# Kernel tuning notes

Measured on AMD Instinct MI355X. Metric: run time of the kernel, lower is better.

The kernel has to match this reference:

```python
import jax, jax.numpy as jnp
import numpy as np

# config constants (init_kwargs)
WC, WS = 0.5, 0.5            # boundary cosine / structural weights (hybrid mode)
TARGET_BPP = 6.0             # target_bytes_per_patch
GAIN = 1.0                   # target_patch_gain
THRESH = 0.5                 # boundary_threshold; mask = p >= THRESH
EPS = 1e-6

_POP6 = jnp.array([bin(i).count('1') for i in range(64)], dtype=jnp.int32)

def _pop6(x):
    return _POP6[jnp.clip(x, 0, 63)]

def _logit(p):
    p = jnp.clip(p, EPS, 1.0 - EPS)
    return jnp.log(p) - jnp.log1p(-p)

def _next(x):  # shift-left by one, zero-padded at end (matches torch q_next pattern)
    return jnp.concatenate([x[1:], jnp.zeros((1,), x.dtype)])

def _hist(vals, mask, bins):
    idx = jnp.where(mask, vals, bins)  # invalid -> out of range, dropped
    return jnp.zeros((bins,), jnp.int32).at[idx].add(1, mode='drop')


def setup_inputs() -> dict:
    key = jax.random.key(0)
    ks = jax.random.split(key, 6)
    B, S = 4, 1048576
    return {
        'boundary_logprobs': jax.random.normal(ks[0], (B, S), jnp.float32),
        'states': jax.random.randint(ks[1], (B, S), 0, 4096, jnp.int32),
        'q_class': jax.random.randint(ks[2], (B, S), 0, 64, jnp.int32),
        'family': jax.random.randint(ks[3], (B, S), 0, 4, jnp.int32),
        'micro_ref': jax.random.randint(ks[4], (B, S), 0, 64, jnp.int32),
        'valid_mask': jax.random.randint(ks[5], (B, S), 0, 2, jnp.int32).astype(bool),
    }


def reference(boundary_logprobs, states, q_class, family, micro_ref, valid_mask):
    B, S = valid_mask.shape
    v = valid_mask.reshape(-1)
    st = states.reshape(-1).astype(jnp.int32)
    q = q_class.reshape(-1).astype(jnp.int32)
    fam = family.reshape(-1).astype(jnp.int32)
    mic = micro_ref.reshape(-1).astype(jnp.int32)

    # --- structural boundary probs ---
    omega12 = st & 0xFFF
    c6 = ((omega12 >> 6) ^ omega12) & 63          # chirality6
    d_chi = jnp.clip(_pop6(c6 ^ _next(c6)).astype(jnp.float32) / 6.0, 0.0, 1.0)
    d_q = _pop6((q & 63) ^ (_next(q) & 63)).astype(jnp.float32) / 6.0
    fx = (fam & 3) ^ (_next(fam) & 3)
    d_fam = (((fx & 1) != 0).astype(jnp.float32) + ((fx & 2) != 0).astype(jnp.float32)) / 2.0
    score = jnp.clip(0.5 * d_chi + 0.35 * d_q + 0.15 * d_fam, EPS, 1.0)
    structural = jnp.where(v, score, 0.0)

    # --- combine with cosine probs (hybrid mode) ---
    cosine = jnp.exp(jnp.minimum(boundary_logprobs.reshape(-1), 0.0))
    combined = (WC * cosine + WS * structural) / max(WC + WS, 1e-6)

    # --- target bytes-per-patch rate adjustment ---
    vf = v.astype(jnp.float32)
    vc = jnp.maximum(jnp.sum(vf), 1.0)
    cur = jnp.clip(jnp.sum(combined * vf) / vc, 1e-4, 1.0 - 1e-4)
    tgt = max(1e-4, min(1.0 - 1e-4, 1.0 / TARGET_BPP))
    shift = _logit(jnp.asarray(tgt, jnp.float32)) - _logit(cur)
    combined = jax.nn.sigmoid(_logit(combined) + GAIN * shift)
    combined = jnp.clip(combined, EPS, 1.0 - EPS)
    combined_logprobs = jnp.log(combined)
    bmask = combined_logprobs >= jnp.log(jnp.asarray(THRESH, jnp.float32))

    # --- histograms over effective (valid) positions ---
    shell = _pop6(c6)
    q_hist64 = _hist(q, v, 64)
    family_hist4 = _hist(fam, v, 4)
    micro_hist64 = _hist(mic, v, 64)
    shell_hist7 = _hist(shell, v, 7)
    wt_q = _pop6(q & 63)
    q_weight_hist7 = _hist(wt_q, v, 7)
    bits = ((q & 63)[:, None] >> jnp.arange(6)) & 1            # [n, 6]
    bit_excitation6 = jnp.sum(bits * v[:, None].astype(jnp.int32), axis=0)

    # --- patch lengths (vectorized run-length over valid bytes) ---
    bv = bmask & v
    pos = jnp.cumsum(v.astype(jnp.int32))                      # 1-indexed valid position
    bpos = jnp.where(bv, pos, 0)
    prev = jax.lax.cummax(jnp.concatenate([jnp.zeros((1,), jnp.int32), bpos[:-1]]))
    lengths = jnp.where(bv, pos - prev, 0)                     # dense run lengths at boundaries
    total_valid = pos[-1]
    trailing = total_valid - jax.lax.cummax(bpos)[-1]          # open trailing run
    patch_count = jnp.sum(bv).astype(jnp.int32) + (trailing > 0).astype(jnp.int32)

    return (combined_logprobs.reshape(B, S), bmask.reshape(B, S), structural.reshape(B, S),
            q_hist64, family_hist4, micro_hist64, shell_hist7, q_weight_hist7,
            bit_excitation6, lengths, trailing, patch_count)
```

## Files before the change

kernel.cpp:

```cpp
#include <hip/hip_runtime.h>

#define TPB 256
#define EPT 8
#define CHUNK (TPB * EPT)
#define P2T 1024
#define NSLICE 64

typedef unsigned long long ull;

__device__ __forceinline__ ull shfl_down_u64(ull x, int off) {
    unsigned lo = (unsigned)x, hi = (unsigned)(x >> 32);
    lo = __shfl_down(lo, off, 64);
    hi = __shfl_down(hi, off, 64);
    return ((ull)hi << 32) | lo;
}

__global__ __launch_bounds__(TPB, 4) void k_pass1(
    const float* __restrict__ blp, const int* __restrict__ st,
    const int* __restrict__ q, const int* __restrict__ fam,
    const int* __restrict__ mic, const int* __restrict__ vm,
    float* __restrict__ out_structural,
    int* __restrict__ blocksum_v, double* __restrict__ blocksum_c,
    int* __restrict__ ghist, int n)
{
    __shared__ int lh2[512];
    __shared__ int slhs[24];
    __shared__ int swv[4];
    __shared__ float swc[4];
    for (int t = threadIdx.x; t < 512; t += TPB) lh2[t] = 0;
    if (threadIdx.x < 24) slhs[threadIdx.x] = 0;
    __syncthreads();

    const int tid = threadIdx.x, lane = tid & 63, wave = tid >> 6;
    const long i0 = (long)blockIdx.x * CHUNK + (long)tid * EPT;
    const bool fast = ((long)(blockIdx.x + 1) * CHUNK <= n);

    int stv[9], qv[9], fv[9], micv[8], vmv[8];
    float bpv[8];
    if (fast) {
        const int4 sa = *(const int4*)(st + i0),  sb = *(const int4*)(st + i0 + 4);
        const int4 qa = *(const int4*)(q + i0),   qb = *(const int4*)(q + i0 + 4);
        const int4 fa = *(const int4*)(fam + i0), fb = *(const int4*)(fam + i0 + 4);
        const int4 ma = *(const int4*)(mic + i0), mb = *(const int4*)(mic + i0 + 4);
        const int4 va = *(const int4*)(vm + i0),  vb = *(const int4*)(vm + i0 + 4);
        const float4 ba = *(const float4*)(blp + i0), bb = *(const float4*)(blp + i0 + 4);
        int nst = __shfl_down(sa.x, 1, 64);
        int nq  = __shfl_down(qa.x, 1, 64);
        int nf  = __shfl_down(fa.x, 1, 64);
        if (lane == 63) {
            const long j = i0 + 8;
            nst = (j < n) ? st[j]  : 0;
            nq  = (j < n) ? q[j]   : 0;
            nf  = (j < n) ? fam[j] : 0;
        }
        stv[0]=sa.x; stv[1]=sa.y; stv[2]=sa.z; stv[3]=sa.w; stv[4]=sb.x; stv[5]=sb.y; stv[6]=sb.z; stv[7]=sb.w; stv[8]=nst;
        qv[0]=qa.x;  qv[1]=qa.y;  qv[2]=qa.z;  qv[3]=qa.w;  qv[4]=qb.x;  qv[5]=qb.y;  qv[6]=qb.z;  qv[7]=qb.w;  qv[8]=nq;
        fv[0]=fa.x;  fv[1]=fa.y;  fv[2]=fa.z;  fv[3]=fa.w;  fv[4]=fb.x;  fv[5]=fb.y;  fv[6]=fb.z;  fv[7]=fb.w;  fv[8]=nf;
        micv[0]=ma.x; micv[1]=ma.y; micv[2]=ma.z; micv[3]=ma.w; micv[4]=mb.x; micv[5]=mb.y; micv[6]=mb.z; micv[7]=mb.w;
        vmv[0]=va.x; vmv[1]=va.y; vmv[2]=va.z; vmv[3]=va.w; vmv[4]=vb.x; vmv[5]=vb.y; vmv[6]=vb.z; vmv[7]=vb.w;
        bpv[0]=ba.x; bpv[1]=ba.y; bpv[2]=ba.z; bpv[3]=ba.w; bpv[4]=bb.x; bpv[5]=bb.y; bpv[6]=bb.z; bpv[7]=bb.w;
    } else {
        #pragma unroll
        for (int e = 0; e < 8; ++e) {
            long ii = i0 + e;
            bool r = ii < n;
            stv[e] = r ? st[ii] : 0;  qv[e] = r ? q[ii] : 0;  fv[e] = r ? fam[ii] : 0;
            micv[e] = r ? mic[ii] : 0; vmv[e] = r ? vm[ii] : 0; bpv[e] = r ? blp[ii] : 0.f;
        }
        stv[8] = (i0 + 8 < n) ? st[i0 + 8] : 0;
        qv[8]  = (i0 + 8 < n) ? q[i0 + 8] : 0;
        fv[8]  = (i0 + 8 < n) ? fam[i0 + 8] : 0;
    }

    int sv = 0;
    float scf = 0.0f;
    ull accF = 0, accS0 = 0, accS1 = 0, accW0 = 0, accW1 = 0, accB = 0;
    float structural[8];
    #pragma unroll
    for (int e = 0; e < 8; ++e) {
        int sti = stv[e], qi = qv[e], fi = fv[e], mi = micv[e];
        int v = (vmv[e] != 0);
        int om  = sti & 0xFFF;      int c6  = ((om  >> 6) ^ om ) & 63;
        int omn = stv[e+1] & 0xFFF; int c6n = ((omn >> 6) ^ omn) & 63;
        float d_chi = (float)__popc(c6 ^ c6n) * (1.0f / 6.0f);
        float d_q   = (float)__popc((qi & 63) ^ (qv[e+1] & 63)) * (1.0f / 6.0f);
        int fx = (fi & 3) ^ (fv[e+1] & 3);
        float d_fam = (float)((fx & 1) + ((fx >> 1) & 1)) * 0.5f;
        float score = 0.5f * d_chi + 0.35f * d_q + 0.15f * d_fam;
        score = fminf(fmaxf(score, 1e-6f), 1.0f);
        structural[e] = v ? score : 0.0f;
        float cosine = expf(fminf(bpv[e], 0.0f));
        float combined = 0.5f * (cosine + structural[e]);
        if (v) {
            sv += 1;
            scf += combined;
            atomicAdd(&lh2[(wave << 6) + (qi & 63)], 1);
            atomicAdd(&lh2[256 + (wave << 6) + (mi & 63)], 1);
            accF += 1ULL << ((fi & 3) * 16);
            int sh = __popc(c6);
            ull ts = 1ULL << ((sh & 3) * 16);
            if (sh < 4) accS0 += ts; else accS1 += ts;
            int wq = __popc(qi & 63);
            ull tw = 1ULL << ((wq & 3) * 16);
            if (wq < 4) accW0 += tw; else accW1 += tw;
            accB += ((ull)(qi & 63) * 0x0000201008040201ULL) & 0x0004010040100401ULL;
        }
    }

    if (fast) {
        float4 o;
        o.x=structural[0]; o.y=structural[1]; o.z=structural[2]; o.w=structural[3];
        *(float4*)(out_structural + i0) = o;
        o.x=structural[4]; o.y=structural[5]; o.z=structural[6]; o.w=structural[7];
        *(float4*)(out_structural + i0 + 4) = o;
    } else {
        #pragma unroll
        for (int e = 0; e < 8; ++e)
            if (i0 + e < n) out_structural[i0 + e] = structural[e];
    }

    #pragma unroll
    for (int off = 32; off > 0; off >>= 1) {
        sv  += __shfl_down(sv, off, 64);
        scf += __shfl_down(scf, off, 64);
        accF  += shfl_down_u64(accF, off);
        accS0 += shfl_down_u64(accS0, off);
        accS1 += shfl_down_u64(accS1, off);
        accW0 += shfl_down_u64(accW0, off);
        accW1 += shfl_down_u64(accW1, off);
        accB  += shfl_down_u64(accB, off);
    }
    if (lane == 0) {
        swv[wave] = sv; swc[wave] = scf;
        #pragma unroll
        for (int b2 = 0; b2 < 4; ++b2) atomicAdd(&slhs[b2],      (int)((accF  >> (16*b2)) & 0xFFFF));
        #pragma unroll
        for (int b2 = 0; b2 < 4; ++b2) atomicAdd(&slhs[4 + b2],  (int)((accS0 >> (16*b2)) & 0xFFFF));
        #pragma unroll
        for (int b2 = 0; b2 < 3; ++b2) atomicAdd(&slhs[8 + b2],  (int)((accS1 >> (16*b2)) & 0xFFFF));
        #pragma unroll
        for (int b2 = 0; b2 < 4; ++b2) atomicAdd(&slhs[11 + b2], (int)((accW0 >> (16*b2)) & 0xFFFF));
        #pragma unroll
        for (int b2 = 0; b2 < 3; ++b2) atomicAdd(&slhs[15 + b2], (int)((accW1 >> (16*b2)) & 0xFFFF));
        #pragma unroll
        for (int b2 = 0; b2 < 6; ++b2) atomicAdd(&slhs[18 + b2], (int)((accB  >> (10*b2)) & 0x3FF));
    }
    __syncthreads();
    if (tid == 0) {
        blocksum_v[blockIdx.x] = swv[0] + swv[1] + swv[2] + swv[3];
        blocksum_c[blockIdx.x] = (double)swc[0] + (double)swc[1] + (double)swc[2] + (double)swc[3];
    }
    int* gh = ghist + (blockIdx.x & (NSLICE - 1)) * 152;
    for (int t2 = tid; t2 < 152; t2 += TPB) {
        int val;
        if (t2 < 64)        val = lh2[t2] + lh2[64 + t2] + lh2[128 + t2] + lh2[192 + t2];
        else if (t2 < 68)   val = slhs[t2 - 64];
        else if (t2 < 132) { int b2 = t2 - 68; val = lh2[256 + b2] + lh2[320 + b2] + lh2[384 + b2] + lh2[448 + b2]; }
        else if (t2 < 139)  val = slhs[4 + (t2 - 132)];
        else if (t2 < 146)  val = slhs[11 + (t2 - 139)];
        else                val = slhs[18 + (t2 - 146)];
        if (val) atomicAdd(&gh[t2], val);
    }
}

__global__ __launch_bounds__(P2T) void k_pass2(
    const int* __restrict__ bsv, const double* __restrict__ bsc, int nb,
    int* __restrict__ pos_offset, float* __restrict__ shiftp,
    int* __restrict__ totalv_p, const int* __restrict__ ghist,
    float* __restrict__ out_hist)
{
    __shared__ int s[P2T];
    __shared__ double d[P2T];
    int t = threadIdx.x;
    int c0 = 2 * t, c1 = 2 * t + 1;
    int v0 = (c0 < nb) ? bsv[c0] : 0;
    int v1 = (c1 < nb) ? bsv[c1] : 0;
    double x0 = (c0 < nb) ? bsc[c0] : 0.0;
    double x1 = (c1 < nb) ? bsc[c1] : 0.0;
    s[t] = v0 + v1; d[t] = x0 + x1;
    __syncthreads();
    for (int off = 1; off < P2T; off <<= 1) {
        int add = (t >= off) ? s[t - off] : 0;
        __syncthreads();
        s[t] += add;
        __syncthreads();
    }
    if (c0 < nb) pos_offset[c0] = s[t] - v0 - v1;
    if (c1 < nb) pos_offset[c1] = s[t] - v1;
    for (int off = P2T / 2; off > 0; off >>= 1) {
        if (t < off) d[t] += d[t + off];
        __syncthreads();
    }
    if (t == 0) {
        int total_v = s[P2T - 1];
        *totalv_p = total_v;
        double vc = (double)(total_v > 1 ? total_v : 1);
        float cur = (float)(d[0] / vc);
        cur = fminf(fmaxf(cur, 1e-4f), 0.9999f);
        float p = fminf(fmaxf(cur, 1e-6f), 0.999999f);
        float lc = logf(p) - log1pf(-p);
        float tgt = (float)(1.0 / 6.0);
        float lt = logf(tgt) - log1pf(-tgt);
        *shiftp = lt - lc;
    }
    if (t < 152) {
        int acc = 0;
        #pragma unroll 8
        for (int sl = 0; sl < NSLICE; ++sl) acc += ghist[sl * 152 + t];
        out_hist[t] = (float)acc;
    }
}

__global__ __launch_bounds__(TPB, 8) void k_pass3(
    const float* __restrict__ strc, const float* __restrict__ blp,
    const float* __restrict__ shiftp, const int* __restrict__ pos_offset,
    float* __restrict__ out_logp, float* __restrict__ out_bmask,
    float* __restrict__ out_len, int* __restrict__ chunk_cnt,
    int* __restrict__ chunk_last, ull* __restrict__ chunk_first, int n)
{
    __shared__ int swt[4], swm[4], scnt[4];
    __shared__ ull sfirst[4];
    const int tid = threadIdx.x, lane = tid & 63, wave = tid >> 6;
    const long i0 = (long)blockIdx.x * CHUNK + (long)tid * EPT;
    const bool fast = ((long)(blockIdx.x + 1) * CHUNK <= n);
    const float shift = *shiftp;

    float sv8[8], bp8[8];
    if (fast) {
        const float4 s0 = *(const float4*)(strc + i0), s1 = *(const float4*)(strc + i0 + 4);
        const float4 p0 = *(const float4*)(blp + i0),  p1 = *(const float4*)(blp + i0 + 4);
        sv8[0]=s0.x; sv8[1]=s0.y; sv8[2]=s0.z; sv8[3]=s0.w; sv8[4]=s1.x; sv8[5]=s1.y; sv8[6]=s1.z; sv8[7]=s1.w;
        bp8[0]=p0.x; bp8[1]=p0.y; bp8[2]=p0.z; bp8[3]=p0.w; bp8[4]=p1.x; bp8[5]=p1.y; bp8[6]=p1.z; bp8[7]=p1.w;
    } else {
        #pragma unroll
        for (int e = 0; e < 8; ++e) {
            long ii = i0 + e;
            bool r = ii < n;
            sv8[e] = r ? strc[ii] : 0.0f;
            bp8[e] = r ? blp[ii] : 0.0f;
        }
    }

    unsigned mv = 0, mb = 0;
    float lp[8], bmf[8], lenv[8];
    #pragma unroll
    for (int e = 0; e < 8; ++e) {
        float s = sv8[e];
        int v = (s > 0.0f);
        float cosine = expf(fminf(bp8[e], 0.0f));
        float comb = 0.5f * (cosine + s);
        float p = fminf(fmaxf(comb, 1e-6f), 0.999999f);
        float z = logf(p) - log1pf(-p) + shift;
        float sgm = 1.0f / (1.0f + expf(-z));
        sgm = fminf(fmaxf(sgm, 1e-6f), 0.999999f);
        float clp = logf(sgm);
        lp[e] = clp;
        int bm = (clp >= -0.69314718f) ? 1 : 0;
        bmf[e] = (float)bm;
        mv |= (unsigned)v << e;
        if (bm & v) mb |= 1u << e;
        lenv[e] = 0.0f;
    }
    if (fast) {
        float4 o;
        o.x=lp[0]; o.y=lp[1]; o.z=lp[2]; o.w=lp[3];     *(float4*)(out_logp + i0) = o;
        o.x=lp[4]; o.y=lp[5]; o.z=lp[6]; o.w=lp[7];     *(float4*)(out_logp + i0 + 4) = o;
        o.x=bmf[0]; o.y=bmf[1]; o.z=bmf[2]; o.w=bmf[3]; *(float4*)(out_bmask + i0) = o;
        o.x=bmf[4]; o.y=bmf[5]; o.z=bmf[6]; o.w=bmf[7]; *(float4*)(out_bmask + i0 + 4) = o;
    } else {
        #pragma unroll
        for (int e = 0; e < 8; ++e)
            if (i0 + e < n) { out_logp[i0 + e] = lp[e]; out_bmask[i0 + e] = bmf[e]; }
    }

    int tvc = __popc(mv);
    int x = tvc;
    #pragma unroll
    for (int off = 1; off < 64; off <<= 1) {
        int y = __shfl_up(x, off, 64);
        if (lane >= off) x += y;
    }
    if (lane == 63) swt[wave] = x;
    __syncthreads();
    int wb = pos_offset[blockIdx.x];
    for (int w2 = 0; w2 < wave; ++w2) wb += swt[w2];
    const int vbase = wb + (x - tvc);

    int last = -1;
    if (mb) {
        int hb = 31 - __clz(mb);
        last = vbase + __popc(mv & ((2u << hb) - 1));
    }
    int m = last;
    #pragma unroll
    for (int off = 1; off < 64; off <<= 1) {
        int y = __shfl_up(m, off, 64);
        if (lane >= off && y > m) m = y;
    }
    int exm = __shfl_up(m, 1, 64);
    if (lane == 0) exm = -1;
    if (lane == 63) swm[wave] = m;
    int cnt = __popc(mb);
    ull fp = ~0ULL;
    if (mb) {
        int lb = __ffs(mb) - 1;
        int fv2 = vbase + __popc(mv & ((2u << lb) - 1));
        fp = ((ull)(unsigned)(i0 + lb) << 32) | (unsigned)fv2;
    }
    #pragma unroll
    for (int off = 32; off > 0; off >>= 1) {
        cnt += __shfl_down(cnt, off, 64);
        ull fo = shfl_down_u64(fp, off);
        if (fo < fp) fp = fo;
    }
    if (lane == 0) { scnt[wave] = cnt; sfirst[wave] = fp; }
    __syncthreads();

    int prev = exm;
    for (int w2 = 0; w2 < wave; ++w2) if (swm[w2] > prev) prev = swm[w2];
    int runv = 0;
    #pragma unroll
    for (int e = 0; e < 8; ++e) {
        runv += (mv >> e) & 1;
        if ((mb >> e) & 1) {
            int pos = vbase + runv;
            lenv[e] = (prev >= 0) ? (float)(pos - prev) : 0.0f;
            prev = pos;
        }
    }
    if (fast) {
        float4 o;
        o.x=lenv[0]; o.y=lenv[1]; o.z=lenv[2]; o.w=lenv[3]; *(float4*)(out_len + i0) = o;
        o.x=lenv[4]; o.y=lenv[5]; o.z=lenv[6]; o.w=lenv[7]; *(float4*)(out_len + i0 + 4) = o;
    } else {
        #pragma unroll
        for (int e = 0; e < 8; ++e)
            if (i0 + e < n) out_len[i0 + e] = lenv[e];
    }
    if (tid == 0) {
        int c = scnt[0] + scnt[1] + scnt[2] + scnt[3];
        int L = swm[0];
        if (swm[1] > L) L = swm[1];
        if (swm[2] > L) L = swm[2];
        if (swm[3] > L) L = swm[3];
        ull F = sfirst[0];
        if (sfirst[1] < F) F = sfirst[1];
        if (sfirst[2] < F) F = sfirst[2];
        if (sfirst[3] < F) F = sfirst[3];
        chunk_cnt[blockIdx.x] = c;
        chunk_last[blockIdx.x] = L > 0 ? L : 0;
        chunk_first[blockIdx.x] = F;
    }
}

__global__ __launch_bounds__(P2T) void k_pass4(
    const int* __restrict__ chunk_cnt, const int* __restrict__ chunk_last,
    const ull* __restrict__ chunk_first, const int* __restrict__ totalv_p,
    int nb, float* __restrict__ out_len,
    float* __restrict__ out_trailing, float* __restrict__ out_patch)
{
    __shared__ int s[P2T];
    __shared__ int cs[P2T];
    int t = threadIdx.x;
    int c0 = 2 * t, c1 = 2 * t + 1;
    int a = 0, b = 0;
    if (c0 < nb) { int z = chunk_last[c0]; a = z > 0 ? z : 0; }
    if (c1 < nb) { int z = chunk_last[c1]; b = z > 0 ? z : 0; }
    int cnt = ((c0 < nb) ? chunk_cnt[c0] : 0) + ((c1 < nb) ? chunk_cnt[c1] : 0);
    s[t] = a > b ? a : b;
    cs[t] = cnt;
    __syncthreads();
    for (int off = 1; off < P2T; off <<= 1) {
        int y = (t >= off) ? s[t - off] : 0;
        __syncthreads();
        if (y > s[t]) s[t] = y;
        __syncthreads();
    }
    int excl = (t > 0) ? s[t - 1] : 0;
    int carry0 = excl;
    int carry1 = excl > a ? excl : a;
    if (c0 < nb) {
        ull F = chunk_first[c0];
        if (F != ~0ULL) {
            int fi = (int)(F >> 32);
            int fv2 = (int)(F & 0xFFFFFFFFu);
            out_len[fi] = (float)(fv2 - carry0);
        }
    }
    if (c1 < nb) {
        ull F = chunk_first[c1];
        if (F != ~0ULL) {
            int fi = (int)(F >> 32);
            int fv2 = (int)(F & 0xFFFFFFFFu);
            out_len[fi] = (float)(fv2 - carry1);
        }
    }
    int gmax = s[P2T - 1];
    __syncthreads();
    for (int off = P2T / 2; off > 0; off >>= 1) {
        if (t < off) cs[t] += cs[t + off];
        __syncthreads();
    }
    if (t == 0) {
        int total_v = *totalv_p;
        int trailing = total_v - gmax;
        int patch = cs[0] + (trailing > 0 ? 1 : 0);
        *out_trailing = (float)trailing;
        *out_patch = (float)patch;
    }
}

extern "C" void kernel_launch(void* const* d_in, const int* in_sizes, int n_in,
                              void* d_out, int out_size, void* d_ws, size_t ws_size,
                              hipStream_t stream)
{
    const float* blp = (const float*)d_in[0];
    const int* st   = (const int*)d_in[1];
    const int* q    = (const int*)d_in[2];
    const int* fam  = (const int*)d_in[3];
    const int* mic  = (const int*)d_in[4];
    const int* vm   = (const int*)d_in[5];
    const int n = in_sizes[0];
    const int nb = (n + CHUNK - 1) / CHUNK;

    float* out = (float*)d_out;
    float* out_logp       = out;
    float* out_bmask      = out + (size_t)n;
    float* out_structural = out + 2 * (size_t)n;
    float* out_hist       = out + 3 * (size_t)n;
    float* out_len        = out + 3 * (size_t)n + 152;
    float* out_trailing   = out + 4 * (size_t)n + 152;
    float* out_patch      = out + 4 * (size_t)n + 153;

    char* w = (char*)d_ws;
    int*    ghist      = (int*)(w);
    int*    blocksum_v = (int*)(w + 40960);
    int*    pos_offset = (int*)(w + 57344);
    int*    chunk_cnt  = (int*)(w + 73728);
    int*    chunk_last = (int*)(w + 90112);
    float*  shiftp     = (float*)(w + 106496);
    int*    totalv_p   = (int*)(w + 106500);
    double* blocksum_c = (double*)(w + 110592);
    ull*    chunk_first= (ull*)(w + 131072);

    hipMemsetAsync(ghist, 0, NSLICE * 152 * 4, stream);

    k_pass1<<<dim3(nb), dim3(TPB), 0, stream>>>(
        blp, st, q, fam, mic, vm, out_structural,
        blocksum_v, blocksum_c, ghist, n);

    k_pass2<<<dim3(1), dim3(P2T), 0, stream>>>(
        blocksum_v, blocksum_c, nb, pos_offset, shiftp, totalv_p,
        ghist, out_hist);

    k_pass3<<<dim3(nb), dim3(TPB), 0, stream>>>(
        out_structural, blp, shiftp, pos_offset, out_logp, out_bmask,
        out_len, chunk_cnt, chunk_last, chunk_first, n);

    k_pass4<<<dim3(1), dim3(P2T), 0, stream>>>(
        chunk_cnt, chunk_last, chunk_first, totalv_p, nb, out_len,
        out_trailing, out_patch);
}
```

Baseline: 194.5 us.

## Fold single-block scan passes into last-block and decoupled-lookback logic

```diff
diff --git a/kernel.cpp b/kernel.cpp
--- a/kernel.cpp
+++ b/kernel.cpp
@@ -3,7 +3,6 @@
 #define TPB 256
 #define EPT 8
 #define CHUNK (TPB * EPT)
-#define P2T 1024
 #define NSLICE 64
 
 typedef unsigned long long ull;
@@ -14,21 +13,35 @@
     hi = __shfl_down(hi, off, 64);
     return ((ull)hi << 32) | lo;
 }
+__device__ __forceinline__ int aload32(int* p) {
+    return __hip_atomic_load(p, __ATOMIC_RELAXED, __HIP_MEMORY_SCOPE_AGENT);
+}
+__device__ __forceinline__ ull aload64(ull* p) {
+    return __hip_atomic_load(p, __ATOMIC_RELAXED, __HIP_MEMORY_SCOPE_AGENT);
+}
+__device__ __forceinline__ void astore64(ull* p, ull v) {
+    __hip_atomic_store(p, v, __ATOMIC_RELAXED, __HIP_MEMORY_SCOPE_AGENT);
+}
 
 __global__ __launch_bounds__(TPB, 4) void k_pass1(
     const float* __restrict__ blp, const int* __restrict__ st,
     const int* __restrict__ q, const int* __restrict__ fam,
     const int* __restrict__ mic, const int* __restrict__ vm,
     float* __restrict__ out_structural,
-    int* __restrict__ blocksum_v, double* __restrict__ blocksum_c,
-    int* __restrict__ ghist, int n)
+    int* __restrict__ bsum_v, ull* __restrict__ bsum_c,
+    int* __restrict__ ghist, int* __restrict__ ctrl,
+    int* __restrict__ pos_offset, float* __restrict__ shiftp,
+    int* __restrict__ totalv_p, float* __restrict__ out_hist, int n, int nb)
 {
     __shared__ int lh2[512];
-    __shared__ int slhs[24];
+    __shared__ int slhs[11];
     __shared__ int swv[4];
     __shared__ float swc[4];
+    __shared__ int sLast;
+    __shared__ int escan[TPB];
+    __shared__ double edbl[TPB];
     for (int t = threadIdx.x; t < 512; t += TPB) lh2[t] = 0;
-    if (threadIdx.x < 24) slhs[threadIdx.x] = 0;
+    if (threadIdx.x < 11) slhs[threadIdx.x] = 0;
     __syncthreads();
 
     const int tid = threadIdx.x, lane = tid & 63, wave = tid >> 6;
@@ -74,7 +87,7 @@
 
     int sv = 0;
     float scf = 0.0f;
-    ull accF = 0, accS0 = 0, accS1 = 0, accW0 = 0, accW1 = 0, accB = 0;
+    ull accF = 0, accS0 = 0, accS1 = 0;
     float structural[8];
     #pragma unroll
     for (int e = 0; e < 8; ++e) {
@@ -100,10 +113,6 @@
             int sh = __popc(c6);
             ull ts = 1ULL << ((sh & 3) * 16);
             if (sh < 4) accS0 += ts; else accS1 += ts;
-            int wq = __popc(qi & 63);
-            ull tw = 1ULL << ((wq & 3) * 16);
-            if (wq < 4) accW0 += tw; else accW1 += tw;
-            accB += ((ull)(qi & 63) * 0x0000201008040201ULL) & 0x0004010040100401ULL;
         }
     }
 
@@ -126,76 +135,75 @@
         accF  += shfl_down_u64(accF, off);
         accS0 += shfl_down_u64(accS0, off);
         accS1 += shfl_down_u64(accS1, off);
-        accW0 += shfl_down_u64(accW0, off);
-        accW1 += shfl_down_u64(accW1, off);
-        accB  += shfl_down_u64(accB, off);
     }
     if (lane == 0) {
         swv[wave] = sv; swc[wave] = scf;
         #pragma unroll
-        for (int b2 = 0; b2 < 4; ++b2) atomicAdd(&slhs[b2],      (int)((accF  >> (16*b2)) & 0xFFFF));
-        #pragma unroll
-        for (int b2 = 0; b2 < 4; ++b2) atomicAdd(&slhs[4 + b2],  (int)((accS0 >> (16*b2)) & 0xFFFF));
-        #pragma unroll
-        for (int b2 = 0; b2 < 3; ++b2) atomicAdd(&slhs[8 + b2],  (int)((accS1 >> (16*b2)) & 0xFFFF));
-        #pragma unroll
-        for (int b2 = 0; b2 < 4; ++b2) atomicAdd(&slhs[11 + b2], (int)((accW0 >> (16*b2)) & 0xFFFF));
-        #pragma unroll
-        for (int b2 = 0; b2 < 3; ++b2) atomicAdd(&slhs[15 + b2], (int)((accW1 >> (16*b2)) & 0xFFFF));
-        #pragma unroll
-        for (int b2 = 0; b2 < 6; ++b2) atomicAdd(&slhs[18 + b2], (int)((accB  >> (10*b2)) & 0x3FF));
+        for (int b2 = 0; b2 < 4; ++b2) atomicAdd(&slhs[b2],     (int)((accF  >> (16*b2)) & 0xFFFF));
+        #pragma unroll
+        for (int b2 = 0; b2 < 4; ++b2) atomicAdd(&slhs[4 + b2], (int)((accS0 >> (16*b2)) & 0xFFFF));
+        #pragma unroll
+        for (int b2 = 0; b2 < 3; ++b2) atomicAdd(&slhs[8 + b2], (int)((accS1 >> (16*b2)) & 0xFFFF));
     }
     __syncthreads();
     if (tid == 0) {
-        blocksum_v[blockIdx.x] = swv[0] + swv[1] + swv[2] + swv[3];
-        blocksum_c[blockIdx.x] = (double)swc[0] + (double)swc[1] + (double)swc[2] + (double)swc[3];
+        int bv = swv[0] + swv[1] + swv[2] + swv[3];
+        double bc = (double)swc[0] + (double)swc[1] + (double)swc[2] + (double)swc[3];
+        atomicExch(&bsum_v[blockIdx.x], bv);
+        atomicExch(&bsum_c[blockIdx.x], __double_as_longlong(bc));
     }
     int* gh = ghist + (blockIdx.x & (NSLICE - 1)) * 152;
-    for (int t2 = tid; t2 < 152; t2 += TPB) {
+    for (int t2 = tid; t2 < 139; t2 += TPB) {
         int val;
         if (t2 < 64)        val = lh2[t2] + lh2[64 + t2] + lh2[128 + t2] + lh2[192 + t2];
         else if (t2 < 68)   val = slhs[t2 - 64];
-        else if (t2 < 132) { int b2 = t2 - 68; val = lh2[256 + b2] + lh2[320 + b2] + lh2[384 + b2] + lh2[448 + b2]; }
-        else if (t2 < 139)  val = slhs[4 + (t2 - 132)];
-        else if (t2 < 146)  val = slhs[11 + (t2 - 139)];
-        else                val = slhs[18 + (t2 - 146)];
+        else if (t2 < 132) { int b2 = t2 - 68; val = lh2[128 + 128 + b2] + lh2[256 + 64 + b2] + lh2[384 + b2] + lh2[448 + b2]; }
+        else                val = slhs[4 + (t2 - 132)];
         if (val) atomicAdd(&gh[t2], val);
     }
-}
-
-__global__ __launch_bounds__(P2T) void k_pass2(
-    const int* __restrict__ bsv, const double* __restrict__ bsc, int nb,
-    int* __restrict__ pos_offset, float* __restrict__ shiftp,
-    int* __restrict__ totalv_p, const int* __restrict__ ghist,
-    float* __restrict__ out_hist)
-{
-    __shared__ int s[P2T];
-    __shared__ double d[P2T];
-    int t = threadIdx.x;
-    int c0 = 2 * t, c1 = 2 * t + 1;
-    int v0 = (c0 < nb) ? bsv[c0] : 0;
-    int v1 = (c1 < nb) ? bsv[c1] : 0;
-    double x0 = (c0 < nb) ? bsc[c0] : 0.0;
-    double x1 = (c1 < nb) ? bsc[c1] : 0.0;
-    s[t] = v0 + v1; d[t] = x0 + x1;
-    __syncthreads();
-    for (int off = 1; off < P2T; off <<= 1) {
-        int add = (t >= off) ? s[t - off] : 0;
+
+    __syncthreads();
+    if (tid == 0) sLast = (atomicAdd(&ctrl[0], 1) == nb - 1);
+    __syncthreads();
+    if (!sLast) return;
+
+    const int G = (nb + TPB - 1) / TPB;
+    int myv[16];
+    int msum = 0;
+    double myd = 0.0;
+    for (int g = 0; g < G; ++g) {
+        int j = tid * G + g;
+        int v = 0;
+        if (j < nb) {
+            v = aload32(&bsum_v[j]);
+            myd += __longlong_as_double(aload64(&bsum_c[j]));
+        }
+        myv[g] = v;
+        msum += v;
+    }
+    escan[tid] = msum;
+    edbl[tid] = myd;
+    __syncthreads();
+    for (int off = 1; off < TPB; off <<= 1) {
+        int add = (tid >= off) ? escan[tid - off] : 0;
         __syncthreads();
-        s[t] += add;
+        escan[tid] += add;
         __syncthreads();
     }
-    if (c0 < nb) pos_offset[c0] = s[t] - v0 - v1;
-    if (c1 < nb) pos_offset[c1] = s[t] - v1;
-    for (int off = P2T / 2; off > 0; off >>= 1) {
-        if (t < off) d[t] += d[t + off];
+    int run = escan[tid] - msum;
+    for (int g = 0; g < G; ++g) {
+        int j = tid * G + g;
+        if (j < nb) { pos_offset[j] = run; run += myv[g]; }
+    }
+    for (int off = TPB / 2; off > 0; off >>= 1) {
+        if (tid < off) edbl[tid] += edbl[tid + off];
         __syncthreads();
     }
-    if (t == 0) {
-        int total_v = s[P2T - 1];
+    if (tid == 0) {
+        int total_v = escan[TPB - 1];
         *totalv_p = total_v;
         double vc = (double)(total_v > 1 ? total_v : 1);
-        float cur = (float)(d[0] / vc);
+        float cur = (float)(edbl[0] / vc);
         cur = fminf(fmaxf(cur, 1e-4f), 0.9999f);
         float p = fminf(fmaxf(cur, 1e-6f), 0.999999f);
         float lc = logf(p) - log1pf(-p);
@@ -203,11 +211,23 @@
         float lt = logf(tgt) - log1pf(-tgt);
         *shiftp = lt - lc;
     }
-    if (t < 152) {
+    for (int t2 = tid; t2 < 139; t2 += TPB) {
         int acc = 0;
         #pragma unroll 8
-        for (int sl = 0; sl < NSLICE; ++sl) acc += ghist[sl * 152 + t];
-        out_hist[t] = (float)acc;
+        for (int sl = 0; sl < NSLICE; ++sl) acc += aload32(&ghist[sl * 152 + t2]);
+        out_hist[t2] = (float)acc;
+        if (t2 < 64) lh2[t2] = acc;
+    }
+    __syncthreads();
+    if (tid < 7) {
+        int s = 0;
+        for (int b = 0; b < 64; ++b) if (__popc(b) == tid) s += lh2[b];
+        out_hist[139 + tid] = (float)s;
+    }
+    if (tid < 6) {
+        int s = 0;
+        for (int b = 0; b < 64; ++b) s += lh2[b] * ((b >> tid) & 1);
+        out_hist[146 + tid] = (float)s;
     }
 }
 
@@ -215,14 +235,16 @@
     const float* __restrict__ strc, const float* __restrict__ blp,
     const float* __restrict__ shiftp, const int* __restrict__ pos_offset,
     float* __restrict__ out_logp, float* __restrict__ out_bmask,
-    float* __restrict__ out_len, int* __restrict__ chunk_cnt,
-    int* __restrict__ chunk_last, ull* __restrict__ chunk_first, int n)
+    float* __restrict__ out_len, ull* __restrict__ desc,
+    int* __restrict__ ctrl, const int* __restrict__ totalv_p,
+    float* __restrict__ out_trailing, float* __restrict__ out_patch, int n, int nb)
 {
     __shared__ int swt[4], swm[4], scnt[4];
-    __shared__ ull sfirst[4];
+    __shared__ int scarry, sLast;
     const int tid = threadIdx.x, lane = tid & 63, wave = tid >> 6;
-    const long i0 = (long)blockIdx.x * CHUNK + (long)tid * EPT;
-    const bool fast = ((long)(blockIdx.x + 1) * CHUNK <= n);
+    const int b = blockIdx.x;
+    const long i0 = (long)b * CHUNK + (long)tid * EPT;
+    const bool fast = ((long)(b + 1) * CHUNK <= n);
     const float shift = *shiftp;
 
     float sv8[8], bp8[8];
@@ -282,7 +304,7 @@
     }
     if (lane == 63) swt[wave] = x;
     __syncthreads();
-    int wb = pos_offset[blockIdx.x];
+    int wb = pos_offset[b];
     for (int w2 = 0; w2 < wave; ++w2) wb += swt[w2];
     const int vbase = wb + (x - tvc);
 
@@ -301,30 +323,45 @@
     if (lane == 0) exm = -1;
     if (lane == 63) swm[wave] = m;
     int cnt = __popc(mb);
-    ull fp = ~0ULL;
-    if (mb) {
-        int lb = __ffs(mb) - 1;
-        int fv2 = vbase + __popc(mv & ((2u << lb) - 1));
-        fp = ((ull)(unsigned)(i0 + lb) << 32) | (unsigned)fv2;
-    }
-    #pragma unroll
-    for (int off = 32; off > 0; off >>= 1) {
-        cnt += __shfl_down(cnt, off, 64);
-        ull fo = shfl_down_u64(fp, off);
-        if (fo < fp) fp = fo;
-    }
-    if (lane == 0) { scnt[wave] = cnt; sfirst[wave] = fp; }
-    __syncthreads();
-
-    int prev = exm;
+    #pragma unroll
+    for (int off = 32; off > 0; off >>= 1) cnt += __shfl_down(cnt, off, 64);
+    if (lane == 0) scnt[wave] = cnt;
+    __syncthreads();
+
+    if (tid == 0) {
+        int L = swm[0];
+        if (swm[1] > L) L = swm[1];
+        if (swm[2] > L) L = swm[2];
+        if (swm[3] > L) L = swm[3];
+        int hasB = (L >= 0);
+        astore64(&desc[b], (1ULL << 63) | ((ull)hasB << 62) | (unsigned)(hasB ? L : 0));
+        int carry = 0;
+        for (int j = b - 1; j >= 0; ) {
+            ull v = aload64(&desc[j]);
+            if (!(v >> 63)) { __builtin_amdgcn_s_sleep(1); continue; }
+            if ((v >> 62) & 1) { carry = (int)(unsigned)(v & 0xFFFFFFFFu); break; }
+            --j;
+        }
+        scarry = carry;
+        int c = scnt[0] + scnt[1] + scnt[2] + scnt[3];
+        atomicAdd(&ctrl[3], c);
+        if (b == nb - 1) {
+            int incl = hasB ? L : carry;
+            atomicExch(&ctrl[2], incl);
+        }
+    }
+    __syncthreads();
+
+    int prev = scarry;
     for (int w2 = 0; w2 < wave; ++w2) if (swm[w2] > prev) prev = swm[w2];
+    if (exm > prev) prev = exm;
     int runv = 0;
     #pragma unroll
     for (int e = 0; e < 8; ++e) {
         runv += (mv >> e) & 1;
         if ((mb >> e) & 1) {
             int pos = vbase + runv;
-            lenv[e] = (prev >= 0) ? (float)(pos - prev) : 0.0f;
+            lenv[e] = (float)(pos - prev);
             prev = pos;
         }
     }
@@ -337,74 +374,17 @@
         for (int e = 0; e < 8; ++e)
             if (i0 + e < n) out_len[i0 + e] = lenv[e];
     }
+
+    __syncthreads();
+    if (tid == 0) sLast = (atomicAdd(&ctrl[1], 1) == nb - 1);
+    __syncthreads();
+    if (!sLast) return;
     if (tid == 0) {
-        int c = scnt[0] + scnt[1] + scnt[2] + scnt[3];
-        int L = swm[0];
-        if (swm[1] > L) L = swm[1];
-        if (swm[2] > L) L = swm[2];
-        if (swm[3] > L) L = swm[3];
-        ull F = sfirst[0];
-        if (sfirst[1] < F) F = sfirst[1];
-        if (sfirst[2] < F) F = sfirst[2];
-        if (sfirst[3] < F) F = sfirst[3];
-        chunk_cnt[blockIdx.x] = c;
-        chunk_last[blockIdx.x] = L > 0 ? L : 0;
-        chunk_first[blockIdx.x] = F;
-    }
-}
-
-__global__ __launch_bounds__(P2T) void k_pass4(
-    const int* __restrict__ chunk_cnt, const int* __restrict__ chunk_last,
-    const ull* __restrict__ chunk_first, const int* __restrict__ totalv_p,
-    int nb, float* __restrict__ out_len,
-    float* __restrict__ out_trailing, float* __restrict__ out_patch)
-{
-    __shared__ int s[P2T];
-    __shared__ int cs[P2T];
-    int t = threadIdx.x;
-    int c0 = 2 * t, c1 = 2 * t + 1;
-    int a = 0, b = 0;
-    if (c0 < nb) { int z = chunk_last[c0]; a = z > 0 ? z : 0; }
-    if (c1 < nb) { int z = chunk_last[c1]; b = z > 0 ? z : 0; }
-    int cnt = ((c0 < nb) ? chunk_cnt[c0] : 0) + ((c1 < nb) ? chunk_cnt[c1] : 0);
-    s[t] = a > b ? a : b;
-    cs[t] = cnt;
-    __syncthreads();
-    for (int off = 1; off < P2T; off <<= 1) {
-        int y = (t >= off) ? s[t - off] : 0;
-        __syncthreads();
-        if (y > s[t]) s[t] = y;
-        __syncthreads();
-    }
-    int excl = (t > 0) ? s[t - 1] : 0;
-    int carry0 = excl;
-    int carry1 = excl > a ? excl : a;
-    if (c0 < nb) {
-        ull F = chunk_first[c0];
-        if (F != ~0ULL) {
-            int fi = (int)(F >> 32);
-            int fv2 = (int)(F & 0xFFFFFFFFu);
-            out_len[fi] = (float)(fv2 - carry0);
-        }
-    }
-    if (c1 < nb) {
-        ull F = chunk_first[c1];
-        if (F != ~0ULL) {
-            int fi = (int)(F >> 32);
-            int fv2 = (int)(F & 0xFFFFFFFFu);
-            out_len[fi] = (float)(fv2 - carry1);
-        }
-    }
-    int gmax = s[P2T - 1];
-    __syncthreads();
-    for (int off = P2T / 2; off > 0; off >>= 1) {
-        if (t < off) cs[t] += cs[t + off];
-        __syncthreads();
-    }
-    if (t == 0) {
+        int gmax = aload32(&ctrl[2]);
+        int gcnt = aload32(&ctrl[3]);
         int total_v = *totalv_p;
         int trailing = total_v - gmax;
-        int patch = cs[0] + (trailing > 0 ? 1 : 0);
+        int patch = gcnt + (trailing > 0 ? 1 : 0);
         *out_trailing = (float)trailing;
         *out_patch = (float)patch;
     }
@@ -433,31 +413,23 @@
     float* out_patch      = out + 4 * (size_t)n + 153;
 
     char* w = (char*)d_ws;
-    int*    ghist      = (int*)(w);
-    int*    blocksum_v = (int*)(w + 40960);
-    int*    pos_offset = (int*)(w + 57344);
-    int*    chunk_cnt  = (int*)(w + 73728);
-    int*    chunk_last = (int*)(w + 90112);
-    float*  shiftp     = (float*)(w + 106496);
-    int*    totalv_p   = (int*)(w + 106500);
-    double* blocksum_c = (double*)(w + 110592);
-    ull*    chunk_first= (ull*)(w + 131072);
-
-    hipMemsetAsync(ghist, 0, NSLICE * 152 * 4, stream);
+    int*  ghist  = (int*)(w);
+    ull*  desc   = (ull*)(w + 40960);
+    int*  ctrl   = (int*)(w + 73728);
+    int*  bsum_v = (int*)(w + 81920);
+    ull*  bsum_c = (ull*)(w + 114688);
+    int*  pos_offset = (int*)(w + 147456);
+    float* shiftp    = (float*)(w + 180224);
+    int*   totalv_p  = (int*)(w + 180228);
+
+    hipMemsetAsync(w, 0, 73728 + 64, stream);
 
     k_pass1<<<dim3(nb), dim3(TPB), 0, stream>>>(
         blp, st, q, fam, mic, vm, out_structural,
-        blocksum_v, blocksum_c, ghist, n);
-
-    k_pass2<<<dim3(1), dim3(P2T), 0, stream>>>(
-        blocksum_v, blocksum_c, nb, pos_offset, shiftp, totalv_p,
-        ghist, out_hist);
+        bsum_v, bsum_c, ghist, ctrl,
+        pos_offset, shiftp, totalv_p, out_hist, n, nb);
 
     k_pass3<<<dim3(nb), dim3(TPB), 0, stream>>>(
         out_structural, blp, shiftp, pos_offset, out_logp, out_bmask,
-        out_len, chunk_cnt, chunk_last, chunk_first, n);
-
-    k_pass4<<<dim3(1), dim3(P2T), 0, stream>>>(
-        chunk_cnt, chunk_last, chunk_first, totalv_p, nb, out_len,
-        out_trailing, out_patch);
-}
+        out_len, desc, ctrl, totalv_p, out_trailing, out_patch, n, nb);
+}
```

After: 220.1 us. 13.2% more time.

## Derive q-weight and bit histograms from q histogram; spread LDS histogram rows

Applied to the files above, without the earlier changes.

```diff
diff --git a/kernel.cpp b/kernel.cpp
--- a/kernel.cpp
+++ b/kernel.cpp
@@ -23,13 +23,10 @@
     int* __restrict__ blocksum_v, double* __restrict__ blocksum_c,
     int* __restrict__ ghist, int n)
 {
-    __shared__ int lh2[512];
-    __shared__ int slhs[24];
+    __shared__ int lh2[2048];
+    __shared__ int slhs[11];
     __shared__ int swv[4];
     __shared__ float swc[4];
-    for (int t = threadIdx.x; t < 512; t += TPB) lh2[t] = 0;
-    if (threadIdx.x < 24) slhs[threadIdx.x] = 0;
-    __syncthreads();
 
     const int tid = threadIdx.x, lane = tid & 63, wave = tid >> 6;
     const long i0 = (long)blockIdx.x * CHUNK + (long)tid * EPT;
@@ -72,9 +69,14 @@
         fv[8]  = (i0 + 8 < n) ? fam[i0 + 8] : 0;
     }
 
+    for (int t = tid; t < 2048; t += TPB) lh2[t] = 0;
+    if (tid < 11) slhs[tid] = 0;
+    __syncthreads();
+
+    const int qrow = ((wave << 2) | (lane & 3)) << 6;
     int sv = 0;
     float scf = 0.0f;
-    ull accF = 0, accS0 = 0, accS1 = 0, accW0 = 0, accW1 = 0, accB = 0;
+    ull accF = 0, accS0 = 0, accS1 = 0;
     float structural[8];
     #pragma unroll
     for (int e = 0; e < 8; ++e) {
@@ -94,16 +96,12 @@
         if (v) {
             sv += 1;
             scf += combined;
-            atomicAdd(&lh2[(wave << 6) + (qi & 63)], 1);
-            atomicAdd(&lh2[256 + (wave << 6) + (mi & 63)], 1);
+            atomicAdd(&lh2[qrow + (qi & 63)], 1);
+            atomicAdd(&lh2[1024 + qrow + (mi & 63)], 1);
             accF += 1ULL << ((fi & 3) * 16);
             int sh = __popc(c6);
             ull ts = 1ULL << ((sh & 3) * 16);
             if (sh < 4) accS0 += ts; else accS1 += ts;
-            int wq = __popc(qi & 63);
-            ull tw = 1ULL << ((wq & 3) * 16);
-            if (wq < 4) accW0 += tw; else accW1 += tw;
-            accB += ((ull)(qi & 63) * 0x0000201008040201ULL) & 0x0004010040100401ULL;
         }
     }
 
@@ -126,24 +124,15 @@
         accF  += shfl_down_u64(accF, off);
         accS0 += shfl_down_u64(accS0, off);
         accS1 += shfl_down_u64(accS1, off);
-        accW0 += shfl_down_u64(accW0, off);
-        accW1 += shfl_down_u64(accW1, off);
-        accB  += shfl_down_u64(accB, off);
     }
     if (lane == 0) {
         swv[wave] = sv; swc[wave] = scf;
         #pragma unroll
-        for (int b2 = 0; b2 < 4; ++b2) atomicAdd(&slhs[b2],      (int)((accF  >> (16*b2)) & 0xFFFF));
-        #pragma unroll
-        for (int b2 = 0; b2 < 4; ++b2) atomicAdd(&slhs[4 + b2],  (int)((accS0 >> (16*b2)) & 0xFFFF));
-        #pragma unroll
-        for (int b2 = 0; b2 < 3; ++b2) atomicAdd(&slhs[8 + b2],  (int)((accS1 >> (16*b2)) & 0xFFFF));
-        #pragma unroll
-        for (int b2 = 0; b2 < 4; ++b2) atomicAdd(&slhs[11 + b2], (int)((accW0 >> (16*b2)) & 0xFFFF));
-        #pragma unroll
-        for (int b2 = 0; b2 < 3; ++b2) atomicAdd(&slhs[15 + b2], (int)((accW1 >> (16*b2)) & 0xFFFF));
-        #pragma unroll
-        for (int b2 = 0; b2 < 6; ++b2) atomicAdd(&slhs[18 + b2], (int)((accB  >> (10*b2)) & 0x3FF));
+        for (int b2 = 0; b2 < 4; ++b2) atomicAdd(&slhs[b2],     (int)((accF  >> (16*b2)) & 0xFFFF));
+        #pragma unroll
+        for (int b2 = 0; b2 < 4; ++b2) atomicAdd(&slhs[4 + b2], (int)((accS0 >> (16*b2)) & 0xFFFF));
+        #pragma unroll
+        for (int b2 = 0; b2 < 3; ++b2) atomicAdd(&slhs[8 + b2], (int)((accS1 >> (16*b2)) & 0xFFFF));
     }
     __syncthreads();
     if (tid == 0) {
@@ -151,14 +140,22 @@
         blocksum_c[blockIdx.x] = (double)swc[0] + (double)swc[1] + (double)swc[2] + (double)swc[3];
     }
     int* gh = ghist + (blockIdx.x & (NSLICE - 1)) * 152;
-    for (int t2 = tid; t2 < 152; t2 += TPB) {
+    for (int t2 = tid; t2 < 139; t2 += TPB) {
         int val;
-        if (t2 < 64)        val = lh2[t2] + lh2[64 + t2] + lh2[128 + t2] + lh2[192 + t2];
-        else if (t2 < 68)   val = slhs[t2 - 64];
-        else if (t2 < 132) { int b2 = t2 - 68; val = lh2[256 + b2] + lh2[320 + b2] + lh2[384 + b2] + lh2[448 + b2]; }
-        else if (t2 < 139)  val = slhs[4 + (t2 - 132)];
-        else if (t2 < 146)  val = slhs[11 + (t2 - 139)];
-        else                val = slhs[18 + (t2 - 146)];
+        if (t2 < 64) {
+            val = 0;
+            #pragma unroll
+            for (int r = 0; r < 16; ++r) val += lh2[(r << 6) + t2];
+        } else if (t2 < 68) {
+            val = slhs[t2 - 64];
+        } else if (t2 < 132) {
+            int b2 = t2 - 68;
+            val = 0;
+            #pragma unroll
+            for (int r = 0; r < 16; ++r) val += lh2[1024 + (r << 6) + b2];
+        } else {
+            val = slhs[4 + (t2 - 132)];
+        }
         if (val) atomicAdd(&gh[t2], val);
     }
 }
@@ -171,6 +168,7 @@
 {
     __shared__ int s[P2T];
     __shared__ double d[P2T];
+    __shared__ int qh[64];
     int t = threadIdx.x;
     int c0 = 2 * t, c1 = 2 * t + 1;
     int v0 = (c0 < nb) ? bsv[c0] : 0;
@@ -178,6 +176,13 @@
     double x0 = (c0 < nb) ? bsc[c0] : 0.0;
     double x1 = (c1 < nb) ? bsc[c1] : 0.0;
     s[t] = v0 + v1; d[t] = x0 + x1;
+    if (t < 139) {
+        int acc = 0;
+        #pragma unroll 8
+        for (int sl = 0; sl < NSLICE; ++sl) acc += ghist[sl * 152 + t];
+        out_hist[t] = (float)acc;
+        if (t < 64) qh[t] = acc;
+    }
     __syncthreads();
     for (int off = 1; off < P2T; off <<= 1) {
         int add = (t >= off) ? s[t - off] : 0;
@@ -203,11 +208,15 @@
         float lt = logf(tgt) - log1pf(-tgt);
         *shiftp = lt - lc;
     }
-    if (t < 152) {
-        int acc = 0;
-        #pragma unroll 8
-        for (int sl = 0; sl < NSLICE; ++sl) acc += ghist[sl * 152 + t];
-        out_hist[t] = (float)acc;
+    if (t < 7) {
+        int sacc = 0;
+        for (int b = 0; b < 64; ++b) if (__popc(b) == t) sacc += qh[b];
+        out_hist[139 + t] = (float)sacc;
+    }
+    if (t < 6) {
+        int sacc = 0;
+        for (int b = 0; b < 64; ++b) sacc += qh[b] * ((b >> t) & 1);
+        out_hist[146 + t] = (float)sacc;
     }
 }
 
```

New measurement: 192.0 us. Within noise of the previous version (-1.2%).
